# Performance work log

Hardware: AMD Instinct MI355X
Metric: run time of the kernel (lower is better)

The kernel has to match this reference:

```python
import jax, jax.numpy as jnp
import numpy as np

B, S, D, K = 2048, 200, 64, 4  # batch, seq_len, dim, num_interest


def setup_inputs() -> dict:
    key = jax.random.key(0)
    k1, k2, k3, k4 = jax.random.split(key, 4)
    item_his_emb = jax.random.normal(k1, (B, S, D), dtype=jnp.float32)
    item_eb = jax.random.normal(k2, (B, D), dtype=jnp.float32)
    mask = jax.random.randint(k3, (B, S), 0, 2, dtype=jnp.int32)
    W = jax.random.normal(k4, (D, K * D), dtype=jnp.float32) * 0.05
    b = jnp.zeros((K * D,), dtype=jnp.float32)
    return {"item_his_emb": item_his_emb, "item_eb": item_eb, "mask": mask, "W": W, "b": b}


def _squash(v):
    # v: [B, K, D]; squash nonlinearity with the module's epsilon
    n2 = jnp.sum(jnp.square(v), axis=-1, keepdims=True)
    return (n2 / (1.0 + n2) / jnp.sqrt(n2 + 1e-9)) * v


def reference(item_his_emb, item_eb, mask, W, b):
    # bilinear_type == 1: Dense(dim * num_interest)
    hat = item_his_emb @ W + b                      # [B, S, K*D]
    hat = hat.reshape(B, S, K, D).transpose(0, 2, 1, 3)  # [B, K, S, D]

    mask_zero = (mask == 0)[:, None, :]             # [B, 1, S] broadcast over K
    cw = jnp.zeros((B, K, S), dtype=item_his_emb.dtype)

    interest = None
    for i in range(3):
        sw = jax.nn.softmax(cw, axis=1)             # softmax over interests
        sw = jnp.where(mask_zero, 0.0, sw)          # [B, K, S]
        interest = _squash(jnp.einsum('bks,bksd->bkd', sw, hat))  # [B, K, D]
        if i < 2:
            cw = cw + jnp.einsum('bksd,bkd->bks', hat, interest)

    # readout: softmax attention over interests against target item, hard argmax gather
    atten = jax.nn.softmax(jnp.einsum('bkd,bd->bk', interest, item_eb), axis=1)
    idx = jnp.argmax(atten, axis=1)                 # [B]
    readout = jnp.take_along_axis(interest, idx[:, None, None], axis=1)[:, 0, :]  # [B, D]
    return interest, readout
```

## Files before the change

kernel.cpp:

```cpp
#include <hip/hip_runtime.h>


#define NB 2048
#define NS 200
#define ND 64
#define NK 4
#define NT 512

__device__ __forceinline__ float wred64(float v) {
#pragma unroll
  for (int o = 1; o < 64; o <<= 1) v += __shfl_xor(v, o, 64);
  return v;
}

__device__ __forceinline__ void gload16(const float* g_, float* l_) {
  __builtin_amdgcn_global_load_lds(
      (const __attribute__((address_space(1))) unsigned int*)g_,
      (__attribute__((address_space(3))) unsigned int*)l_, 16, 0, 0);
}

#define RED_GRP(v)                 \
  v += __shfl_xor(v, 16, 64);      \
  v += __shfl_xor(v, 32, 64);

__global__ __launch_bounds__(NT, 4) void caps_kernel(
    const float* __restrict__ his, const float* __restrict__ itemeb,
    const int* __restrict__ mask, const float* __restrict__ W,
    const float* __restrict__ bias, float* __restrict__ out) {
  __shared__ float semb[NS * ND];
  __shared__ float upool[2048];
  __shared__ float se[NK][ND];
  __shared__ float pv[NK][ND];
  __shared__ float sG[NK][ND];
  __shared__ float su[NK][ND];
  __shared__ float smsk[NS];
  __shared__ float pts[8][NK];
  __shared__ float sts[NK];
  __shared__ float soff[NK];
  __shared__ float satt[NK];
  __shared__ int sidx;

  const int t = threadIdx.x;
  const int w = t >> 6, l = t & 63;
  const int g = l >> 4, j = l & 15;
  const int gid = (w << 2) | g;
  const int k = w & 3, h = w >> 2;
  const int b = blockIdx.x;
  const float* eb = his + (size_t)b * NS * ND;

  for (int i = w; i < 50; i += 8) {
    int s = 4 * i + g;
    int q = (j - s) & 15;
    gload16(eb + (s << 6) + (q << 2), &semb[i * 256]);
  }
  float wreg[32];
#pragma unroll
  for (int c = 0; c < 32; ++c)
    wreg[c] = W[(size_t)(32 * h + c) * (NK * ND) + k * ND + l];
  float breg = bias[k * ND + l];
  float iq = itemeb[(size_t)b * ND + l];
  if (t < NS) smsk[t] = (mask[b * NS + t] != 0) ? 1.0f : 0.0f;
  __syncthreads();

  for (int it = 0; it < 3; ++it) {
    if (it > 0) {
      if (w < 4) {
        const float4* Wr = (const float4*)(W + (size_t)l * (NK * ND) + w * ND);
        const float4* Gk = (const float4*)&sG[w][0];
        float a = 0.f;
#pragma unroll
        for (int d4 = 0; d4 < 16; ++d4) {
          float4 wv = Wr[d4], gv = Gk[d4];
          a += wv.x * gv.x + wv.y * gv.y + wv.z * gv.z + wv.w * gv.w;
        }
        su[w][l] = a;
      } else {
        float ob = wred64(breg * sG[w - 4][l]);
        if (l == 0) soff[w - 4] = ob;
      }
      __syncthreads();

      if (t < NS) {
        float lg0 = soff[0], lg1 = soff[1], lg2 = soff[2], lg3 = soff[3];
#pragma unroll
        for (int jj = 0; jj < 16; ++jj) {
          float4 eq = *(const float4*)&semb[(t << 6) + 4 * ((jj + t) & 15)];
          float4 u0 = *(const float4*)&su[0][4 * jj];
          float4 u1 = *(const float4*)&su[1][4 * jj];
          float4 u2 = *(const float4*)&su[2][4 * jj];
          float4 u3 = *(const float4*)&su[3][4 * jj];
          lg0 += eq.x * u0.x + eq.y * u0.y + eq.z * u0.z + eq.w * u0.w;
          lg1 += eq.x * u1.x + eq.y * u1.y + eq.z * u1.z + eq.w * u1.w;
          lg2 += eq.x * u2.x + eq.y * u2.y + eq.z * u2.z + eq.w * u2.w;
          lg3 += eq.x * u3.x + eq.y * u3.y + eq.z * u3.z + eq.w * u3.w;
        }
        float m = fmaxf(fmaxf(lg0, lg1), fmaxf(lg2, lg3));
        float e0 = __expf(lg0 - m), e1 = __expf(lg1 - m);
        float e2 = __expf(lg2 - m), e3 = __expf(lg3 - m);
        float r = smsk[t] / (e0 + e1 + e2 + e3);
        *(float4*)&upool[t * 4] = make_float4(e0 * r, e1 * r, e2 * r, e3 * r);
      }
      __syncthreads();
    }

    float4 a0 = {0, 0, 0, 0}, a1 = {0, 0, 0, 0}, a2 = {0, 0, 0, 0},
           a3 = {0, 0, 0, 0};
    float t0 = 0, t1 = 0, t2 = 0, t3 = 0;
    const int nt_ = (w < 2) ? 7 : 6;
    for (int tt = 0; tt < nt_; ++tt) {
      int s = gid + 32 * tt;
      float4 eq = *(const float4*)&semb[(s << 6) + 4 * ((j + s) & 15)];
      if (it == 0) {
        float swa = 0.25f * smsk[s];
        a0.x += swa * eq.x; a0.y += swa * eq.y;
        a0.z += swa * eq.z; a0.w += swa * eq.w;
        t0 += swa;
      } else {
        float4 s4 = *(const float4*)&upool[s * 4];
        a0.x += s4.x * eq.x; a0.y += s4.x * eq.y; a0.z += s4.x * eq.z; a0.w += s4.x * eq.w;
        a1.x += s4.y * eq.x; a1.y += s4.y * eq.y; a1.z += s4.y * eq.z; a1.w += s4.y * eq.w;
        a2.x += s4.z * eq.x; a2.y += s4.z * eq.y; a2.z += s4.z * eq.z; a2.w += s4.z * eq.w;
        a3.x += s4.w * eq.x; a3.y += s4.w * eq.y; a3.z += s4.w * eq.z; a3.w += s4.w * eq.w;
        t0 += s4.x; t1 += s4.y; t2 += s4.z; t3 += s4.w;
      }
    }
    if (it > 0) __syncthreads();

    RED_GRP(a0.x) RED_GRP(a0.y) RED_GRP(a0.z) RED_GRP(a0.w) RED_GRP(t0)
    if (it > 0) {
      RED_GRP(a1.x) RED_GRP(a1.y) RED_GRP(a1.z) RED_GRP(a1.w)
      RED_GRP(a2.x) RED_GRP(a2.y) RED_GRP(a2.z) RED_GRP(a2.w)
      RED_GRP(a3.x) RED_GRP(a3.y) RED_GRP(a3.z) RED_GRP(a3.w)
      RED_GRP(t1) RED_GRP(t2) RED_GRP(t3)
    }
    if (l < 16) {
      *(float4*)&upool[w * 256 + 4 * l] = a0;
      if (it > 0) {
        *(float4*)&upool[w * 256 + 64 + 4 * l] = a1;
        *(float4*)&upool[w * 256 + 128 + 4 * l] = a2;
        *(float4*)&upool[w * 256 + 192 + 4 * l] = a3;
      }
    }
    if (l == 0) {
      pts[w][0] = t0;
      if (it > 0) { pts[w][1] = t1; pts[w][2] = t2; pts[w][3] = t3; }
    }
    __syncthreads();

    if (w < 4) {
      int kk = (it == 0) ? 0 : w;
      float e = 0.f;
#pragma unroll
      for (int w2 = 0; w2 < 8; ++w2) e += upool[w2 * 256 + kk * 64 + l];
      se[w][l] = e;
      if (l == 0) {
        float s_ = 0.f;
#pragma unroll
        for (int w2 = 0; w2 < 8; ++w2) s_ += pts[w2][kk];
        sts[w] = s_;
      }
    }
    __syncthreads();

    float vp = 0.f;
#pragma unroll
    for (int q2 = 0; q2 < 8; ++q2) {
      float4 e4 = *(const float4*)&se[k][4 * (8 * h + q2)];
      vp += e4.x * wreg[4 * q2 + 0] + e4.y * wreg[4 * q2 + 1] +
            e4.z * wreg[4 * q2 + 2] + e4.w * wreg[4 * q2 + 3];
    }
    if (h == 1) pv[k][l] = vp;
    __syncthreads();

    if (h == 0) {
      float accv = vp + pv[k][l] + sts[k] * breg;
      float n2 = wred64(accv * accv);
      float scale = n2 / (1.f + n2) / sqrtf(n2 + 1e-9f);
      float inter = scale * accv;
      if (it < 2) {
        sG[k][l] = (it == 0) ? inter : (sG[k][l] + inter);
      } else {
        out[((size_t)b * NK + k) * ND + l] = inter;
        float dot = wred64(inter * iq);
        pv[k][l] = inter;
        if (l == 0) satt[k] = dot;
      }
    }
    __syncthreads();
  }

  if (t == 0) {
    int bi = 0;
    float bv = satt[0];
#pragma unroll
    for (int kk = 1; kk < NK; ++kk)
      if (satt[kk] > bv) { bv = satt[kk]; bi = kk; }
    sidx = bi;
  }
  __syncthreads();
  if (t < ND) out[(size_t)NB * NK * ND + (size_t)b * ND + t] = pv[sidx][t];
}

extern "C" void kernel_launch(void* const* d_in, const int* in_sizes, int n_in,
                              void* d_out, int out_size, void* d_ws, size_t ws_size,
                              hipStream_t stream) {
  (void)in_sizes; (void)n_in; (void)out_size; (void)d_ws; (void)ws_size;
  const float* his = (const float*)d_in[0];
  const float* itemeb = (const float*)d_in[1];
  const int* mask = (const int*)d_in[2];
  const float* W = (const float*)d_in[3];
  const float* bias = (const float*)d_in[4];
  float* out = (float*)d_out;
  caps_kernel<<<NB, NT, 0, stream>>>(his, itemeb, mask, W, bias, out);
}
```

Baseline: 96.81 us.

## Compact masked-in positions and stage only active rows in LDS with overflow path

Builds a compacted index list of unmasked sequence positions with a ballot/prefix scan, then stages only those rows (up to a cap of 140) into LDS. Rows past the cap are read straight from global memory. This skips loading and processing masked positions and shrinks LDS use so six blocks per CU can be resident instead of four. It also moves the routing-logit dot products to four threads per row with shuffle reductions, fuses the u/offset computation into the squash stage, and drops the W register cache and some barriers. In exchange it adds scan overhead and a slower global-memory path when more than 140 positions are active.

```diff
diff --git a/kernel.cpp b/kernel.cpp
--- a/kernel.cpp
+++ b/kernel.cpp
@@ -6,6 +6,7 @@
 #define ND 64
 #define NK 4
 #define NT 512
+#define CAP 140
 
 __device__ __forceinline__ float wred64(float v) {
 #pragma unroll
@@ -19,86 +20,108 @@
       (__attribute__((address_space(3))) unsigned int*)l_, 16, 0, 0);
 }
 
-#define RED_GRP(v)                 \
-  v += __shfl_xor(v, 16, 64);      \
-  v += __shfl_xor(v, 32, 64);
-
-__global__ __launch_bounds__(NT, 4) void caps_kernel(
+#define RED_GRP(v) v += __shfl_xor(v, 16, 64); v += __shfl_xor(v, 32, 64);
+#define RED_Q(v)   v += __shfl_xor(v, 1, 64);  v += __shfl_xor(v, 2, 64);
+
+__global__ __launch_bounds__(NT, 6) void caps_kernel(
     const float* __restrict__ his, const float* __restrict__ itemeb,
     const int* __restrict__ mask, const float* __restrict__ W,
     const float* __restrict__ bias, float* __restrict__ out) {
-  __shared__ float semb[NS * ND];
-  __shared__ float upool[2048];
+  __shared__ float semb[(CAP + 4) * ND];
+  __shared__ float ssw4[NS * NK];
+  __shared__ float pe[8][NK][ND];
   __shared__ float se[NK][ND];
   __shared__ float pv[NK][ND];
   __shared__ float sG[NK][ND];
   __shared__ float su[NK][ND];
-  __shared__ float smsk[NS];
+  __shared__ unsigned short sidxs[NS];
+  __shared__ int swofs[8];
   __shared__ float pts[8][NK];
-  __shared__ float sts[NK];
-  __shared__ float soff[NK];
-  __shared__ float satt[NK];
+  __shared__ float soff[NK], satt[NK];
   __shared__ int sidx;
 
   const int t = threadIdx.x;
   const int w = t >> 6, l = t & 63;
   const int g = l >> 4, j = l & 15;
   const int gid = (w << 2) | g;
-  const int k = w & 3, h = w >> 2;
+  const int k_ = w & 3, h_ = w >> 2;
   const int b = blockIdx.x;
   const float* eb = his + (size_t)b * NS * ND;
 
-  for (int i = w; i < 50; i += 8) {
-    int s = 4 * i + g;
-    int q = (j - s) & 15;
-    gload16(eb + (s << 6) + (q << 2), &semb[i * 256]);
+  int m = (t < NS) ? (mask[b * NS + t] != 0) : 0;
+  unsigned long long bal = __ballot(m);
+  int pre = __popcll(bal & ((1ull << l) - 1));
+  if (l == 0) swofs[w] = __popcll(bal);
+  float breg = bias[k_ * ND + l];
+  float iq = itemeb[(size_t)b * ND + l];
+  __syncthreads();
+  int base = 0;
+#pragma unroll
+  for (int ww = 0; ww < 8; ++ww) base += (ww < w) ? swofs[ww] : 0;
+  if (m) sidxs[base + pre] = (unsigned short)t;
+  int nact = 0;
+#pragma unroll
+  for (int ww = 0; ww < 8; ++ww) nact += swofs[ww];
+  __syncthreads();
+  const int ncore = nact < CAP ? nact : CAP;
+
+  for (int i4 = w; 4 * i4 < ncore; i4 += 8) {
+    int i = 4 * i4 + g;
+    int ii = (i < ncore) ? i : (ncore - 1);
+    int s = sidxs[ii];
+    int qq = (j - i) & 15;
+    gload16(eb + (s << 6) + (qq << 2), &semb[i4 * 256]);
   }
-  float wreg[32];
-#pragma unroll
-  for (int c = 0; c < 32; ++c)
-    wreg[c] = W[(size_t)(32 * h + c) * (NK * ND) + k * ND + l];
-  float breg = bias[k * ND + l];
-  float iq = itemeb[(size_t)b * ND + l];
-  if (t < NS) smsk[t] = (mask[b * NS + t] != 0) ? 1.0f : 0.0f;
   __syncthreads();
 
   for (int it = 0; it < 3; ++it) {
     if (it > 0) {
-      if (w < 4) {
-        const float4* Wr = (const float4*)(W + (size_t)l * (NK * ND) + w * ND);
-        const float4* Gk = (const float4*)&sG[w][0];
-        float a = 0.f;
-#pragma unroll
-        for (int d4 = 0; d4 < 16; ++d4) {
-          float4 wv = Wr[d4], gv = Gk[d4];
-          a += wv.x * gv.x + wv.y * gv.y + wv.z * gv.z + wv.w * gv.w;
-        }
-        su[w][l] = a;
-      } else {
-        float ob = wred64(breg * sG[w - 4][l]);
-        if (l == 0) soff[w - 4] = ob;
-      }
-      __syncthreads();
-
-      if (t < NS) {
-        float lg0 = soff[0], lg1 = soff[1], lg2 = soff[2], lg3 = soff[3];
-#pragma unroll
-        for (int jj = 0; jj < 16; ++jj) {
-          float4 eq = *(const float4*)&semb[(t << 6) + 4 * ((jj + t) & 15)];
+      const int qB = t & 3;
+      for (int i = (t >> 2); i < ncore; i += 128) {
+        float l0 = 0.f, l1 = 0.f, l2 = 0.f, l3 = 0.f;
+#pragma unroll
+        for (int c2 = 0; c2 < 4; ++c2) {
+          int jj = qB * 4 + c2;
+          float4 eq = *(const float4*)&semb[(i << 6) + 4 * ((jj + i) & 15)];
           float4 u0 = *(const float4*)&su[0][4 * jj];
           float4 u1 = *(const float4*)&su[1][4 * jj];
           float4 u2 = *(const float4*)&su[2][4 * jj];
           float4 u3 = *(const float4*)&su[3][4 * jj];
-          lg0 += eq.x * u0.x + eq.y * u0.y + eq.z * u0.z + eq.w * u0.w;
-          lg1 += eq.x * u1.x + eq.y * u1.y + eq.z * u1.z + eq.w * u1.w;
-          lg2 += eq.x * u2.x + eq.y * u2.y + eq.z * u2.z + eq.w * u2.w;
-          lg3 += eq.x * u3.x + eq.y * u3.y + eq.z * u3.z + eq.w * u3.w;
+          l0 += eq.x * u0.x + eq.y * u0.y + eq.z * u0.z + eq.w * u0.w;
+          l1 += eq.x * u1.x + eq.y * u1.y + eq.z * u1.z + eq.w * u1.w;
+          l2 += eq.x * u2.x + eq.y * u2.y + eq.z * u2.z + eq.w * u2.w;
+          l3 += eq.x * u3.x + eq.y * u3.y + eq.z * u3.z + eq.w * u3.w;
         }
-        float m = fmaxf(fmaxf(lg0, lg1), fmaxf(lg2, lg3));
-        float e0 = __expf(lg0 - m), e1 = __expf(lg1 - m);
-        float e2 = __expf(lg2 - m), e3 = __expf(lg3 - m);
-        float r = smsk[t] / (e0 + e1 + e2 + e3);
-        *(float4*)&upool[t * 4] = make_float4(e0 * r, e1 * r, e2 * r, e3 * r);
+        RED_Q(l0) RED_Q(l1) RED_Q(l2) RED_Q(l3)
+        l0 += soff[0]; l1 += soff[1]; l2 += soff[2]; l3 += soff[3];
+        float mx = fmaxf(fmaxf(l0, l1), fmaxf(l2, l3));
+        float e0 = __expf(l0 - mx), e1 = __expf(l1 - mx);
+        float e2 = __expf(l2 - mx), e3 = __expf(l3 - mx);
+        float r = 1.0f / (e0 + e1 + e2 + e3);
+        if (qB == 0)
+          *(float4*)&ssw4[i * 4] = make_float4(e0 * r, e1 * r, e2 * r, e3 * r);
+      }
+      for (int i = CAP + t; i < nact; i += NT) {
+        int s = sidxs[i];
+        const float4* er = (const float4*)(eb + (s << 6));
+        float l0 = soff[0], l1 = soff[1], l2 = soff[2], l3 = soff[3];
+#pragma unroll
+        for (int jj = 0; jj < 16; ++jj) {
+          float4 eq = er[jj];
+          float4 u0 = *(const float4*)&su[0][4 * jj];
+          float4 u1 = *(const float4*)&su[1][4 * jj];
+          float4 u2 = *(const float4*)&su[2][4 * jj];
+          float4 u3 = *(const float4*)&su[3][4 * jj];
+          l0 += eq.x * u0.x + eq.y * u0.y + eq.z * u0.z + eq.w * u0.w;
+          l1 += eq.x * u1.x + eq.y * u1.y + eq.z * u1.z + eq.w * u1.w;
+          l2 += eq.x * u2.x + eq.y * u2.y + eq.z * u2.z + eq.w * u2.w;
+          l3 += eq.x * u3.x + eq.y * u3.y + eq.z * u3.z + eq.w * u3.w;
+        }
+        float mx = fmaxf(fmaxf(l0, l1), fmaxf(l2, l3));
+        float e0 = __expf(l0 - mx), e1 = __expf(l1 - mx);
+        float e2 = __expf(l2 - mx), e3 = __expf(l3 - mx);
+        float r = 1.0f / (e0 + e1 + e2 + e3);
+        *(float4*)&ssw4[i * 4] = make_float4(e0 * r, e1 * r, e2 * r, e3 * r);
       }
       __syncthreads();
     }
@@ -106,17 +129,13 @@
     float4 a0 = {0, 0, 0, 0}, a1 = {0, 0, 0, 0}, a2 = {0, 0, 0, 0},
            a3 = {0, 0, 0, 0};
     float t0 = 0, t1 = 0, t2 = 0, t3 = 0;
-    const int nt_ = (w < 2) ? 7 : 6;
-    for (int tt = 0; tt < nt_; ++tt) {
-      int s = gid + 32 * tt;
-      float4 eq = *(const float4*)&semb[(s << 6) + 4 * ((j + s) & 15)];
+    for (int i = gid; i < ncore; i += 32) {
+      float4 eq = *(const float4*)&semb[(i << 6) + 4 * ((j + i) & 15)];
       if (it == 0) {
-        float swa = 0.25f * smsk[s];
-        a0.x += swa * eq.x; a0.y += swa * eq.y;
-        a0.z += swa * eq.z; a0.w += swa * eq.w;
-        t0 += swa;
+        a0.x += eq.x; a0.y += eq.y; a0.z += eq.z; a0.w += eq.w;
+        t0 += 1.0f;
       } else {
-        float4 s4 = *(const float4*)&upool[s * 4];
+        float4 s4 = *(const float4*)&ssw4[i * 4];
         a0.x += s4.x * eq.x; a0.y += s4.x * eq.y; a0.z += s4.x * eq.z; a0.w += s4.x * eq.w;
         a1.x += s4.y * eq.x; a1.y += s4.y * eq.y; a1.z += s4.y * eq.z; a1.w += s4.y * eq.w;
         a2.x += s4.z * eq.x; a2.y += s4.z * eq.y; a2.z += s4.z * eq.z; a2.w += s4.z * eq.w;
@@ -124,69 +143,92 @@
         t0 += s4.x; t1 += s4.y; t2 += s4.z; t3 += s4.w;
       }
     }
-    if (it > 0) __syncthreads();
-
+    for (int i = CAP + gid; i < nact; i += 32) {
+      int s = sidxs[i];
+      float4 eq = *(const float4*)&eb[(s << 6) + 4 * j];
+      if (it == 0) {
+        a0.x += eq.x; a0.y += eq.y; a0.z += eq.z; a0.w += eq.w;
+        t0 += 1.0f;
+      } else {
+        float4 s4 = *(const float4*)&ssw4[i * 4];
+        a0.x += s4.x * eq.x; a0.y += s4.x * eq.y; a0.z += s4.x * eq.z; a0.w += s4.x * eq.w;
+        a1.x += s4.y * eq.x; a1.y += s4.y * eq.y; a1.z += s4.y * eq.z; a1.w += s4.y * eq.w;
+        a2.x += s4.z * eq.x; a2.y += s4.z * eq.y; a2.z += s4.z * eq.z; a2.w += s4.z * eq.w;
+        a3.x += s4.w * eq.x; a3.y += s4.w * eq.y; a3.z += s4.w * eq.z; a3.w += s4.w * eq.w;
+        t0 += s4.x; t1 += s4.y; t2 += s4.z; t3 += s4.w;
+      }
+    }
     RED_GRP(a0.x) RED_GRP(a0.y) RED_GRP(a0.z) RED_GRP(a0.w) RED_GRP(t0)
     if (it > 0) {
       RED_GRP(a1.x) RED_GRP(a1.y) RED_GRP(a1.z) RED_GRP(a1.w)
       RED_GRP(a2.x) RED_GRP(a2.y) RED_GRP(a2.z) RED_GRP(a2.w)
       RED_GRP(a3.x) RED_GRP(a3.y) RED_GRP(a3.z) RED_GRP(a3.w)
       RED_GRP(t1) RED_GRP(t2) RED_GRP(t3)
+    } else {
+      a0.x *= 0.25f; a0.y *= 0.25f; a0.z *= 0.25f; a0.w *= 0.25f;
+      t0 *= 0.25f;
+      a1 = a0; a2 = a0; a3 = a0; t1 = t0; t2 = t0; t3 = t0;
     }
     if (l < 16) {
-      *(float4*)&upool[w * 256 + 4 * l] = a0;
-      if (it > 0) {
-        *(float4*)&upool[w * 256 + 64 + 4 * l] = a1;
-        *(float4*)&upool[w * 256 + 128 + 4 * l] = a2;
-        *(float4*)&upool[w * 256 + 192 + 4 * l] = a3;
-      }
-    }
-    if (l == 0) {
-      pts[w][0] = t0;
-      if (it > 0) { pts[w][1] = t1; pts[w][2] = t2; pts[w][3] = t3; }
-    }
+      *(float4*)&pe[w][0][4 * l] = a0;
+      *(float4*)&pe[w][1][4 * l] = a1;
+      *(float4*)&pe[w][2][4 * l] = a2;
+      *(float4*)&pe[w][3][4 * l] = a3;
+    }
+    if (l == 0) { pts[w][0] = t0; pts[w][1] = t1; pts[w][2] = t2; pts[w][3] = t3; }
     __syncthreads();
 
-    if (w < 4) {
-      int kk = (it == 0) ? 0 : w;
-      float e = 0.f;
-#pragma unroll
-      for (int w2 = 0; w2 < 8; ++w2) e += upool[w2 * 256 + kk * 64 + l];
-      se[w][l] = e;
-      if (l == 0) {
-        float s_ = 0.f;
-#pragma unroll
-        for (int w2 = 0; w2 < 8; ++w2) s_ += pts[w2][kk];
-        sts[w] = s_;
-      }
-    }
-    __syncthreads();
-
-    float vp = 0.f;
-#pragma unroll
-    for (int q2 = 0; q2 < 8; ++q2) {
-      float4 e4 = *(const float4*)&se[k][4 * (8 * h + q2)];
-      vp += e4.x * wreg[4 * q2 + 0] + e4.y * wreg[4 * q2 + 1] +
-            e4.z * wreg[4 * q2 + 2] + e4.w * wreg[4 * q2 + 3];
-    }
-    if (h == 1) pv[k][l] = vp;
-    __syncthreads();
-
-    if (h == 0) {
-      float accv = vp + pv[k][l] + sts[k] * breg;
-      float n2 = wred64(accv * accv);
-      float scale = n2 / (1.f + n2) / sqrtf(n2 + 1e-9f);
-      float inter = scale * accv;
-      if (it < 2) {
-        sG[k][l] = (it == 0) ? inter : (sG[k][l] + inter);
-      } else {
-        out[((size_t)b * NK + k) * ND + l] = inter;
-        float dot = wred64(inter * iq);
-        pv[k][l] = inter;
-        if (l == 0) satt[k] = dot;
-      }
-    }
-    __syncthreads();
+    {
+      int cl = 32 * h_ + (l & 31);
+      float sse = 0.f;
+#pragma unroll
+      for (int w2 = 0; w2 < 8; ++w2) sse += pe[w2][k_][cl];
+      se[k_][cl] = sse;
+      float vp = 0.f;
+      const float* Wc = W + k_ * ND + l;
+#pragma unroll
+      for (int q2 = 0; q2 < 8; ++q2) {
+        int c = 32 * h_ + 4 * q2;
+        float4 e4 = *(const float4*)&se[k_][c];
+        vp += e4.x * Wc[(size_t)(c + 0) * (NK * ND)];
+        vp += e4.y * Wc[(size_t)(c + 1) * (NK * ND)];
+        vp += e4.z * Wc[(size_t)(c + 2) * (NK * ND)];
+        vp += e4.w * Wc[(size_t)(c + 3) * (NK * ND)];
+      }
+      if (h_) pv[k_][l] = vp;
+      __syncthreads();
+
+      if (h_ == 0) {
+        float ts_ = 0.f;
+#pragma unroll
+        for (int w2 = 0; w2 < 8; ++w2) ts_ += pts[w2][k_];
+        float accv = vp + pv[k_][l] + ts_ * breg;
+        float n2 = wred64(accv * accv);
+        float scale = n2 / (1.f + n2) / sqrtf(n2 + 1e-9f);
+        float inter = scale * accv;
+        if (it < 2) {
+          float gnew = (it == 0) ? inter : (sG[k_][l] + inter);
+          sG[k_][l] = gnew;
+          float ob = wred64(breg * gnew);
+          if (l == 0) soff[k_] = ob;
+          const float4* Wr = (const float4*)(W + (size_t)l * (NK * ND) + k_ * ND);
+          const float4* Gk = (const float4*)&sG[k_][0];
+          float a = 0.f;
+#pragma unroll
+          for (int d4 = 0; d4 < 16; ++d4) {
+            float4 wv = Wr[d4], gv = Gk[d4];
+            a += wv.x * gv.x + wv.y * gv.y + wv.z * gv.z + wv.w * gv.w;
+          }
+          su[k_][l] = a;
+        } else {
+          out[((size_t)b * NK + k_) * ND + l] = inter;
+          float dot_ = wred64(inter * iq);
+          pv[k_][l] = inter;
+          if (l == 0) satt[k_] = dot_;
+        }
+      }
+      __syncthreads();
+    }
   }
 
   if (t == 0) {
```

Result: slower. 276.0 us (+185.1%).
